# Kernel optimization log

Measured on AMD Instinct MI355X. Metric: run time of the kernel, lower is better.

Reference implementation:

```python
import jax, jax.numpy as jnp
import numpy as np

K = 3  # Chebyshev filter size (max_view)


def avwgcn(X, E, weights_pool, bias_pool):
    """Adaptive node-wise graph conv. X: [B,N,C_in], E: [N,D]."""
    N = E.shape[0]
    # adaptive adjacency: softmax over rows of relu(E E^T)
    supports = jax.nn.softmax(jax.nn.relu(E @ E.T), axis=1)  # [N,N]
    support_set = [jnp.eye(N, dtype=X.dtype), supports]
    for _ in range(2, K):  # Chebyshev recursion
        support_set.append(2.0 * supports @ support_set[-1] - support_set[-2])
    S = jnp.stack(support_set, axis=0)  # [K,N,N]
    W = jnp.einsum('nd,dkio->nkio', E, weights_pool)  # per-node weights [N,K,Ci,Co]
    bias = E @ bias_pool  # [N,Co]
    XG = jnp.einsum('knm,bmc->bnkc', S, X)  # [B,N,K,Ci]
    return jnp.einsum('bnki,nkio->bno', XG, W) + bias  # [B,N,Co]


def setup_inputs() -> dict:
    key = jax.random.key(0)
    ks = jax.random.split(key, 5)
    B, N, Cin, Cout, D = 32, 4096, 2, 64, 10
    Ci = Cin + Cout  # 66
    X = jax.random.normal(ks[0], (B, N, Cin), dtype=jnp.float32)
    H = jnp.zeros((B, N, Cout), dtype=jnp.float32)
    E = jax.random.normal(ks[1], (N, D), dtype=jnp.float32)
    W_gate = jax.random.normal(ks[2], (D, K, Ci, 2 * Cout), dtype=jnp.float32) * 0.1
    b_gate = jnp.zeros((D, 2 * Cout), dtype=jnp.float32)
    W_update = jax.random.normal(ks[3], (D, K, Ci, Cout), dtype=jnp.float32) * 0.1
    b_update = jnp.zeros((D, Cout), dtype=jnp.float32)
    return {"X": X, "H": H, "E": E, "W_gate": W_gate, "b_gate": b_gate,
            "W_update": W_update, "b_update": b_update}


def reference(X, H, E, W_gate, b_gate, W_update, b_update):
    Cout = H.shape[-1]
    XH = jnp.concatenate([X, H], axis=-1)  # [B,N,Cin+Cout]
    ZR = jax.nn.sigmoid(avwgcn(XH, E, W_gate, b_gate))  # [B,N,2*Cout]
    Z, R = ZR[..., :Cout], ZR[..., Cout:]
    C = jnp.concatenate([X, Z * H], axis=-1)
    HC = jnp.tanh(avwgcn(C, E, W_update, b_update))
    return R * H + (1.0 - R) * HC
```

## Files before the change

kernel.cpp:

```cpp
#include <hip/hip_runtime.h>
#include <math.h>

#define N_NODES 4096
#define BATCH   32
#define D_EMB   10
#define CIN     2
#define COUT    64
#define CI      66
#define KSUP    3
#define NCOLS   2112
#define NPAD    2176
#define LDT     4096

#define KI_REAL 198
#define KILD    232
#define OCH     (32 * KILD)
#define WROW_G  (128 * KILD)
#define WROW_U  (64 * KILD)
#define WGT2_R  (WROW_G + WROW_U)

typedef _Float16 half_t;
typedef __attribute__((ext_vector_type(8))) _Float16 f16x8;
typedef __attribute__((ext_vector_type(4))) _Float16 f16x4;
typedef __attribute__((ext_vector_type(2))) _Float16 f16x2;
typedef __attribute__((ext_vector_type(4))) float f32x4;

union u32h2 { unsigned u; f16x2 h; };

__device__ __forceinline__ float fast_sigmoid(float x) { return 1.f / (1.f + __expf(-x)); }
__device__ __forceinline__ float fast_tanh(float x) { return 1.f - 2.f / (__expf(2.f * x) + 1.f); }

__device__ __forceinline__ void gld_lds16(const half_t* g, half_t* l) {
  __builtin_amdgcn_global_load_lds(
      (const __attribute__((address_space(1))) void*)g,
      (__attribute__((address_space(3))) void*)l, 16, 0, 0);
}

__global__ __launch_bounds__(256) void k_softmax_p(const float* __restrict__ E,
                                                   half_t* __restrict__ Pb) {
  const int n = blockIdx.x;
  const int tid = threadIdx.x;
  __shared__ float En[D_EMB];
  __shared__ float ms[256], ss[256];
  if (tid < D_EMB) En[tid] = E[n * D_EMB + tid];
  __syncthreads();
  float en[D_EMB];
#pragma unroll
  for (int d = 0; d < D_EMB; ++d) en[d] = En[d];

  float m = -1e30f, s = 0.f;
  for (int c = tid; c < N_NODES; c += 256) {
    const float* Ec = E + c * D_EMB;
    float v = 0.f;
#pragma unroll
    for (int d = 0; d < D_EMB; ++d) v += en[d] * Ec[d];
    v = fmaxf(v, 0.f);
    if (v > m) { s *= __expf(m - v); m = v; }
    s += __expf(v - m);
  }
  ms[tid] = m; ss[tid] = s;
  __syncthreads();
  for (int off = 128; off > 0; off >>= 1) {
    if (tid < off) {
      float m2 = ms[tid + off], s2 = ss[tid + off];
      float m1 = ms[tid], s1 = ss[tid];
      float mm = fmaxf(m1, m2);
      ms[tid] = mm;
      ss[tid] = s1 * __expf(m1 - mm) + s2 * __expf(m2 - mm);
    }
    __syncthreads();
  }
  const float M = ms[0];
  const float inv = 1.f / ss[0];
  half_t* Pr = Pb + (size_t)n * N_NODES;
  for (int c = tid; c < N_NODES; c += 256) {
    const float* Ec = E + c * D_EMB;
    float v = 0.f;
#pragma unroll
    for (int d = 0; d < D_EMB; ++d) v += en[d] * Ec[d];
    v = fmaxf(v, 0.f);
    Pr[c] = (half_t)(__expf(v - M) * inv);
  }
}

__global__ __launch_bounds__(256) void k_build_v0(const float* __restrict__ X,
                                                  const float* __restrict__ H,
                                                  half_t* __restrict__ Vt,
                                                  half_t* __restrict__ Vn,
                                                  half_t* __restrict__ Cbt,
                                                  half_t* __restrict__ Cbn) {
  size_t idx = (size_t)blockIdx.x * 256 + threadIdx.x;
  if (idx >= (size_t)N_NODES * NCOLS) return;
  const int m = (int)(idx / NCOLS);
  const int col = (int)(idx % NCOLS);
  const int b = col / CI;
  const int c = col % CI;
  float v;
  if (c < CIN) v = X[((size_t)b * N_NODES + m) * CIN + c];
  else         v = H[((size_t)b * N_NODES + m) * COUT + (c - CIN)];
  const half_t h = (half_t)v;
  Vn[(size_t)m * NPAD + col] = h;
  Vt[(size_t)col * LDT + m] = h;
  if (c < CIN) {
    Cbn[(size_t)m * NPAD + col] = h;
    Cbt[(size_t)col * LDT + m] = h;
  }
}

__device__ __forceinline__ void gemm_compute_tile(const half_t* __restrict__ Lb,
                                                  int wm, int wn, int fofs,
                                                  f32x4 (&acc)[4][4]) {
  const half_t* As_ = Lb;
  const half_t* Bs_ = Lb + 4096;
  f16x8 a[4], b[4];
#pragma unroll
  for (int i = 0; i < 4; ++i)
    a[i] = *(const f16x8*)&As_[((wm >> 4) + i) * 512 + fofs];
#pragma unroll
  for (int j = 0; j < 4; ++j)
    b[j] = *(const f16x8*)&Bs_[((wn >> 4) + j) * 512 + fofs];
  __builtin_amdgcn_s_setprio(1);
#pragma unroll
  for (int i = 0; i < 4; ++i)
#pragma unroll
    for (int j = 0; j < 4; ++j)
      acc[i][j] = __builtin_amdgcn_mfma_f32_16x16x32_f16(a[i], b[j], acc[i][j], 0, 0, 0);
  __builtin_amdgcn_s_setprio(0);
}

__global__ __launch_bounds__(256) void k_gemm_f16(const half_t* __restrict__ A,
                                                  const half_t* __restrict__ Bt,
                                                  half_t* __restrict__ Cn,
                                                  half_t* __restrict__ Ct) {
  __shared__ half_t LB[3][8192];
  const int tid = threadIdx.x;
  const int lane = tid & 63;
  const int wave = tid >> 6;

  int flat = blockIdx.y * 17 + blockIdx.x;
  flat = (flat & 7) * 68 + (flat >> 3);
  const int bx = flat % 17;
  const int by = flat / 17;

  const int wm = (wave >> 1) * 64;
  const int wn = (wave & 1) * 64;
  const int rb = by * 128;
  const int cb = bx * 128;

  const int srow = lane >> 2;
  const int skg = (((lane & 3) + ((lane >> 3) & 3)) & 3) * 8;
  const half_t* ga0 = A + (size_t)(rb + wave * 32 + srow) * N_NODES + skg;
  const half_t* ga1 = ga0 + (size_t)16 * N_NODES;
  const half_t* gb0 = Bt + (size_t)(cb + wave * 32 + srow) * LDT + skg;
  const half_t* gb1 = gb0 + (size_t)16 * LDT;
  const int lA0 = wave * 1024;
  const int lA1 = lA0 + 512;
  const int lB0 = 4096 + wave * 1024;
  const int lB1 = lB0 + 512;

  const int fr = lane & 15;
  const int fg = lane >> 4;
  const int fofs = (4 * fr + ((fg - (fr >> 1)) & 3)) * 8;

  f32x4 acc[4][4] = {};

#define STAGE_T(buf, kk) do { half_t* Lp = LB[(buf)]; \
    gld_lds16(ga0 + (kk), Lp + lA0); gld_lds16(ga1 + (kk), Lp + lA1); \
    gld_lds16(gb0 + (kk), Lp + lB0); gld_lds16(gb1 + (kk), Lp + lB1); } while (0)

  STAGE_T(0, 0);
  STAGE_T(1, 32);

  for (int t = 0; t < 126; t += 3) {
    asm volatile("s_waitcnt vmcnt(4)\n\ts_barrier" ::: "memory");
    STAGE_T(2, (t + 2) * 32);
    gemm_compute_tile(LB[0], wm, wn, fofs, acc);

    asm volatile("s_waitcnt vmcnt(4)\n\ts_barrier" ::: "memory");
    STAGE_T(0, (t + 3) * 32);
    gemm_compute_tile(LB[1], wm, wn, fofs, acc);

    asm volatile("s_waitcnt vmcnt(4)\n\ts_barrier" ::: "memory");
    STAGE_T(1, (t + 4) * 32);
    gemm_compute_tile(LB[2], wm, wn, fofs, acc);
  }
  asm volatile("s_waitcnt vmcnt(4)\n\ts_barrier" ::: "memory");
  gemm_compute_tile(LB[0], wm, wn, fofs, acc);
  asm volatile("s_waitcnt vmcnt(0)\n\ts_barrier" ::: "memory");
  gemm_compute_tile(LB[1], wm, wn, fofs, acc);
#undef STAGE_T

  const int en = lane & 15;
  const int em = (lane >> 4) * 4;
#pragma unroll
  for (int i = 0; i < 4; ++i) {
#pragma unroll
    for (int j = 0; j < 4; ++j) {
      const int m0 = rb + wm + i * 16 + em;
      const int n = cb + wn + j * 16 + en;
      half_t h0 = (half_t)acc[i][j][0];
      half_t h1 = (half_t)acc[i][j][1];
      half_t h2 = (half_t)acc[i][j][2];
      half_t h3 = (half_t)acc[i][j][3];
      if (Ct) {
        f16x4 t4 = {h0, h1, h2, h3};
        *(f16x4*)&Ct[(size_t)n * LDT + m0] = t4;
      }
      Cn[(size_t)(m0 + 0) * NPAD + n] = h0;
      Cn[(size_t)(m0 + 1) * NPAD + n] = h1;
      Cn[(size_t)(m0 + 2) * NPAD + n] = h2;
      Cn[(size_t)(m0 + 3) * NPAD + n] = h3;
    }
  }
}

__global__ __launch_bounds__(256) void k_wgt2(const float* __restrict__ Wg,
                                              const float* __restrict__ Wu,
                                              unsigned* __restrict__ WT2) {
  const int r = blockIdx.x * 256 + threadIdx.x;
  if (r >= WGT2_R) return;
  const float* pool;
  int o, ki, ostr;
  if (r < WROW_G) { o = r / KILD; ki = r % KILD; pool = Wg; ostr = 128; }
  else { int r2 = r - WROW_G; o = r2 / KILD; ki = r2 % KILD; pool = Wu; ostr = 64; }
#pragma unroll
  for (int dp = 0; dp < 5; ++dp) {
    u32h2 v; v.h = f16x2{(half_t)0.f, (half_t)0.f};
    if (ki < KI_REAL) {
      const int k = ki / CI;
      const int i = ki % CI;
      v.h[0] = (half_t)pool[(((size_t)(2 * dp) * KSUP + k) * CI + i) * ostr + o];
      v.h[1] = (half_t)pool[(((size_t)(2 * dp + 1) * KSUP + k) * CI + i) * ostr + o];
    }
    WT2[(size_t)dp * WGT2_R + r] = v.u;
  }
}

__device__ __forceinline__ void stage_xg(const half_t* __restrict__ v0r,
                                         const half_t* __restrict__ g1r,
                                         const half_t* __restrict__ g2r,
                                         half_t* __restrict__ xg, int tid) {
  for (int idx = tid; idx < NCOLS / 8; idx += 256) {
    const f16x8 v0 = *(const f16x8*)&v0r[idx * 8];
    const f16x8 g1 = *(const f16x8*)&g1r[idx * 8];
    const f16x8 g2 = *(const f16x8*)&g2r[idx * 8];
    const f16x8 x2 = g2 + g2 - v0;
#pragma unroll
    for (int e = 0; e < 8; ++e) {
      const int col = idx * 8 + e;
      const int b = col / CI;
      const int i = col - b * CI;
      xg[b * KILD + i] = v0[e];
      xg[b * KILD + CI + i] = g1[e];
      xg[b * KILD + 2 * CI + i] = x2[e];
    }
  }
  for (int z = tid; z < 32 * 17; z += 256) {
    const int b = z / 17;
    const int j = z - b * 17;
    *(unsigned*)&xg[b * KILD + KI_REAL + j * 2] = 0u;
  }
}

__global__ __launch_bounds__(256) void k_gate_t(const half_t* __restrict__ Vn,
                                                const half_t* __restrict__ G1n,
                                                const half_t* __restrict__ G2n,
                                                const unsigned* __restrict__ WT2,
                                                const float* __restrict__ E,
                                                const float* __restrict__ bg,
                                                const float* __restrict__ H,
                                                half_t* __restrict__ Cbn,
                                                half_t* __restrict__ Cbt,
                                                half_t* __restrict__ Rb) {
  const int n0 = blockIdx.x * 2;
  const int tid = threadIdx.x;
  const int lane = tid & 63;
  const int wave = tid >> 6;
  __shared__ half_t Wl[2][OCH];
  __shared__ half_t xg[2][OCH];
  __shared__ float biasl[2][128];

  f16x2 e2p0[5], e2p1[5];
#pragma unroll
  for (int dp = 0; dp < 5; ++dp) {
    e2p0[dp][0] = (half_t)E[n0 * D_EMB + 2 * dp];
    e2p0[dp][1] = (half_t)E[n0 * D_EMB + 2 * dp + 1];
    e2p1[dp][0] = (half_t)E[(n0 + 1) * D_EMB + 2 * dp];
    e2p1[dp][1] = (half_t)E[(n0 + 1) * D_EMB + 2 * dp + 1];
  }

  {
    const int nn = tid >> 7;
    const int o = tid & 127;
    float s = 0.f;
#pragma unroll
    for (int d = 0; d < D_EMB; ++d) s += E[(n0 + nn) * D_EMB + d] * bg[d * 128 + o];
    biasl[nn][o] = s;
  }
  stage_xg(Vn + (size_t)n0 * NPAD, G1n + (size_t)n0 * NPAD, G2n + (size_t)n0 * NPAD, xg[0], tid);
  stage_xg(Vn + (size_t)(n0 + 1) * NPAD, G1n + (size_t)(n0 + 1) * NPAD, G2n + (size_t)(n0 + 1) * NPAD, xg[1], tid);

  const int fr = lane & 15;
  const int fk = (lane >> 4) * 8;
  const int en = lane & 15;
  const int em = (lane >> 4) * 4;
  const int node = wave & 1;
  const int ot = wave >> 1;
  const int nn = n0 + node;

#pragma unroll
  for (int p = 0; p < 4; ++p) {
    if (p > 0) __syncthreads();
    for (int base = tid * 8; base < OCH; base += 2048) {
      float a0[8] = {}, a1[8] = {};
#pragma unroll
      for (int dp = 0; dp < 5; ++dp) {
        const unsigned* wrow = WT2 + (size_t)dp * WGT2_R + p * OCH + base;
        uint4 wa = *(const uint4*)wrow;
        uint4 wb = *(const uint4*)(wrow + 4);
        u32h2 c0, c1, c2, c3;
        c0.u = wa.x; c1.u = wa.y; c2.u = wa.z; c3.u = wa.w;
        a0[0] = __builtin_amdgcn_fdot2(c0.h, e2p0[dp], a0[0], false);
        a0[1] = __builtin_amdgcn_fdot2(c1.h, e2p0[dp], a0[1], false);
        a0[2] = __builtin_amdgcn_fdot2(c2.h, e2p0[dp], a0[2], false);
        a0[3] = __builtin_amdgcn_fdot2(c3.h, e2p0[dp], a0[3], false);
        a1[0] = __builtin_amdgcn_fdot2(c0.h, e2p1[dp], a1[0], false);
        a1[1] = __builtin_amdgcn_fdot2(c1.h, e2p1[dp], a1[1], false);
        a1[2] = __builtin_amdgcn_fdot2(c2.h, e2p1[dp], a1[2], false);
        a1[3] = __builtin_amdgcn_fdot2(c3.h, e2p1[dp], a1[3], false);
        c0.u = wb.x; c1.u = wb.y; c2.u = wb.z; c3.u = wb.w;
        a0[4] = __builtin_amdgcn_fdot2(c0.h, e2p0[dp], a0[4], false);
        a0[5] = __builtin_amdgcn_fdot2(c1.h, e2p0[dp], a0[5], false);
        a0[6] = __builtin_amdgcn_fdot2(c2.h, e2p0[dp], a0[6], false);
        a0[7] = __builtin_amdgcn_fdot2(c3.h, e2p0[dp], a0[7], false);
        a1[4] = __builtin_amdgcn_fdot2(c0.h, e2p1[dp], a1[4], false);
        a1[5] = __builtin_amdgcn_fdot2(c1.h, e2p1[dp], a1[5], false);
        a1[6] = __builtin_amdgcn_fdot2(c2.h, e2p1[dp], a1[6], false);
        a1[7] = __builtin_amdgcn_fdot2(c3.h, e2p1[dp], a1[7], false);
      }
      f16x8 w0, w1;
#pragma unroll
      for (int e = 0; e < 8; ++e) { w0[e] = (half_t)a0[e]; w1[e] = (half_t)a1[e]; }
      *(f16x8*)&Wl[0][base] = w0;
      *(f16x8*)&Wl[1][base] = w1;
    }
    __syncthreads();

    f32x4 acc2[2] = {};
#pragma unroll
    for (int ks = 0; ks < 7; ++ks) {
      const f16x8 a0 = *(const f16x8*)&xg[node][fr * KILD + ks * 32 + fk];
      const f16x8 a1 = *(const f16x8*)&xg[node][(16 + fr) * KILD + ks * 32 + fk];
      const f16x8 b0 = *(const f16x8*)&Wl[node][(ot * 16 + fr) * KILD + ks * 32 + fk];
      acc2[0] = __builtin_amdgcn_mfma_f32_16x16x32_f16(a0, b0, acc2[0], 0, 0, 0);
      acc2[1] = __builtin_amdgcn_mfma_f32_16x16x32_f16(a1, b0, acc2[1], 0, 0, 0);
    }
    const int o_g = p * 32 + ot * 16 + en;
    const float bo = biasl[node][o_g];
#pragma unroll
    for (int i = 0; i < 2; ++i)
#pragma unroll
      for (int r = 0; r < 4; ++r) {
        const int b = i * 16 + em + r;
        const float s = fast_sigmoid(acc2[i][r] + bo);
        if (p < 2) {
          const float hv = H[((size_t)b * N_NODES + nn) * COUT + o_g];
          const half_t z = (half_t)(s * hv);
          const int c0 = b * CI + CIN + o_g;
          Cbn[(size_t)nn * NPAD + c0] = z;
          Cbt[(size_t)c0 * LDT + nn] = z;
        } else {
          Rb[((size_t)b * N_NODES + nn) * COUT + (o_g - 64)] = (half_t)s;
        }
      }
  }
}

__global__ __launch_bounds__(256) void k_update_t(const half_t* __restrict__ Cbn,
                                                  const half_t* __restrict__ G1n,
                                                  const half_t* __restrict__ G2n,
                                                  const unsigned* __restrict__ WT2,
                                                  const float* __restrict__ E,
                                                  const float* __restrict__ bu,
                                                  const float* __restrict__ H,
                                                  const half_t* __restrict__ Rb,
                                                  float* __restrict__ Out) {
  const int n0 = blockIdx.x * 2;
  const int tid = threadIdx.x;
  const int lane = tid & 63;
  const int wave = tid >> 6;
  __shared__ half_t Wl[2][OCH];
  __shared__ half_t xg[2][OCH];
  __shared__ float biasl[2][64];

  f16x2 e2p0[5], e2p1[5];
#pragma unroll
  for (int dp = 0; dp < 5; ++dp) {
    e2p0[dp][0] = (half_t)E[n0 * D_EMB + 2 * dp];
    e2p0[dp][1] = (half_t)E[n0 * D_EMB + 2 * dp + 1];
    e2p1[dp][0] = (half_t)E[(n0 + 1) * D_EMB + 2 * dp];
    e2p1[dp][1] = (half_t)E[(n0 + 1) * D_EMB + 2 * dp + 1];
  }

  if (tid < 128) {
    const int nn = tid >> 6;
    const int o = tid & 63;
    float s = 0.f;
#pragma unroll
    for (int d = 0; d < D_EMB; ++d) s += E[(n0 + nn) * D_EMB + d] * bu[d * COUT + o];
    biasl[nn][o] = s;
  }
  stage_xg(Cbn + (size_t)n0 * NPAD, G1n + (size_t)n0 * NPAD, G2n + (size_t)n0 * NPAD, xg[0], tid);
  stage_xg(Cbn + (size_t)(n0 + 1) * NPAD, G1n + (size_t)(n0 + 1) * NPAD, G2n + (size_t)(n0 + 1) * NPAD, xg[1], tid);

  const int fr = lane & 15;
  const int fk = (lane >> 4) * 8;
  const int en = lane & 15;
  const int em = (lane >> 4) * 4;
  const int node = wave & 1;
  const int ot = wave >> 1;
  const int nn = n0 + node;

#pragma unroll
  for (int p = 0; p < 2; ++p) {
    if (p > 0) __syncthreads();
    for (int base = tid * 8; base < OCH; base += 2048) {
      float a0[8] = {}, a1[8] = {};
#pragma unroll
      for (int dp = 0; dp < 5; ++dp) {
        const unsigned* wrow = WT2 + (size_t)dp * WGT2_R + WROW_G + p * OCH + base;
        uint4 wa = *(const uint4*)wrow;
        uint4 wb = *(const uint4*)(wrow + 4);
        u32h2 c0, c1, c2, c3;
        c0.u = wa.x; c1.u = wa.y; c2.u = wa.z; c3.u = wa.w;
        a0[0] = __builtin_amdgcn_fdot2(c0.h, e2p0[dp], a0[0], false);
        a0[1] = __builtin_amdgcn_fdot2(c1.h, e2p0[dp], a0[1], false);
        a0[2] = __builtin_amdgcn_fdot2(c2.h, e2p0[dp], a0[2], false);
        a0[3] = __builtin_amdgcn_fdot2(c3.h, e2p0[dp], a0[3], false);
        a1[0] = __builtin_amdgcn_fdot2(c0.h, e2p1[dp], a1[0], false);
        a1[1] = __builtin_amdgcn_fdot2(c1.h, e2p1[dp], a1[1], false);
        a1[2] = __builtin_amdgcn_fdot2(c2.h, e2p1[dp], a1[2], false);
        a1[3] = __builtin_amdgcn_fdot2(c3.h, e2p1[dp], a1[3], false);
        c0.u = wb.x; c1.u = wb.y; c2.u = wb.z; c3.u = wb.w;
        a0[4] = __builtin_amdgcn_fdot2(c0.h, e2p0[dp], a0[4], false);
        a0[5] = __builtin_amdgcn_fdot2(c1.h, e2p0[dp], a0[5], false);
        a0[6] = __builtin_amdgcn_fdot2(c2.h, e2p0[dp], a0[6], false);
        a0[7] = __builtin_amdgcn_fdot2(c3.h, e2p0[dp], a0[7], false);
        a1[4] = __builtin_amdgcn_fdot2(c0.h, e2p1[dp], a1[4], false);
        a1[5] = __builtin_amdgcn_fdot2(c1.h, e2p1[dp], a1[5], false);
        a1[6] = __builtin_amdgcn_fdot2(c2.h, e2p1[dp], a1[6], false);
        a1[7] = __builtin_amdgcn_fdot2(c3.h, e2p1[dp], a1[7], false);
      }
      f16x8 w0, w1;
#pragma unroll
      for (int e = 0; e < 8; ++e) { w0[e] = (half_t)a0[e]; w1[e] = (half_t)a1[e]; }
      *(f16x8*)&Wl[0][base] = w0;
      *(f16x8*)&Wl[1][base] = w1;
    }
    __syncthreads();

    f32x4 acc2[2] = {};
#pragma unroll
    for (int ks = 0; ks < 7; ++ks) {
      const f16x8 a0 = *(const f16x8*)&xg[node][fr * KILD + ks * 32 + fk];
      const f16x8 a1 = *(const f16x8*)&xg[node][(16 + fr) * KILD + ks * 32 + fk];
      const f16x8 b0 = *(const f16x8*)&Wl[node][(ot * 16 + fr) * KILD + ks * 32 + fk];
      acc2[0] = __builtin_amdgcn_mfma_f32_16x16x32_f16(a0, b0, acc2[0], 0, 0, 0);
      acc2[1] = __builtin_amdgcn_mfma_f32_16x16x32_f16(a1, b0, acc2[1], 0, 0, 0);
    }
    const int o = p * 32 + ot * 16 + en;
    const float bo = biasl[node][o];
#pragma unroll
    for (int i = 0; i < 2; ++i)
#pragma unroll
      for (int r = 0; r < 4; ++r) {
        const int b = i * 16 + em + r;
        const float hc = fast_tanh(acc2[i][r] + bo);
        const size_t base = ((size_t)b * N_NODES + nn) * COUT + o;
        const float hv = H[base];
        const float rr = (float)Rb[base];
        Out[base] = rr * hv + (1.f - rr) * hc;
      }
  }
}

extern "C" void kernel_launch(void* const* d_in, const int* in_sizes, int n_in,
                              void* d_out, int out_size, void* d_ws, size_t ws_size,
                              hipStream_t stream) {
  const float* X  = (const float*)d_in[0];
  const float* H  = (const float*)d_in[1];
  const float* E  = (const float*)d_in[2];
  const float* Wg = (const float*)d_in[3];
  const float* bg = (const float*)d_in[4];
  const float* Wu = (const float*)d_in[5];
  const float* bu = (const float*)d_in[6];
  float* out = (float*)d_out;

  const size_t SZ_P = (size_t)N_NODES * N_NODES;
  const size_t SZ_M = (size_t)NPAD * LDT;
  half_t* Pb  = (half_t*)d_ws;
  half_t* Vt  = Pb + SZ_P;
  half_t* Vn  = Vt + SZ_M;
  half_t* G1t = Vn + SZ_M;
  half_t* G1n = G1t + SZ_M;
  half_t* G2n = G1n + SZ_M;
  half_t* Cbt = G2n + SZ_M;
  half_t* Cbn = Cbt + SZ_M;
  half_t* Rb  = Cbn + SZ_M;
  unsigned* WT2 = (unsigned*)(Rb + (size_t)BATCH * N_NODES * COUT);

  k_softmax_p<<<N_NODES, 256, 0, stream>>>(E, Pb);
  {
    const size_t tot = (size_t)N_NODES * NCOLS;
    k_build_v0<<<(int)((tot + 255) / 256), 256, 0, stream>>>(X, H, Vt, Vn, Cbt, Cbn);
  }
  k_wgt2<<<(WGT2_R + 255) / 256, 256, 0, stream>>>(Wg, Wu, WT2);

  dim3 gg(NPAD / 128, N_NODES / 128);
  k_gemm_f16<<<gg, 256, 0, stream>>>(Pb, Vt, G1n, G1t);
  k_gemm_f16<<<gg, 256, 0, stream>>>(Pb, G1t, G2n, nullptr);
  k_gate_t<<<N_NODES / 2, 256, 0, stream>>>(Vn, G1n, G2n, WT2, E, bg, H, Cbn, Cbt, Rb);
  k_gemm_f16<<<gg, 256, 0, stream>>>(Pb, Cbt, G1n, G1t);
  k_gemm_f16<<<gg, 256, 0, stream>>>(Pb, G1t, G2n, nullptr);
  k_update_t<<<N_NODES / 2, 256, 0, stream>>>(Cbn, G1n, G2n, WT2, E, bu, H, Rb, out);
}
```

Baseline: 802.8 us.

## Vectorize xg staging with 72-wide K sections and double gate/update block size

Reorders the per-node K dimension into three 72-wide sections (66 real plus padding), so staging the Chebyshev inputs into shared memory uses 8-half vector loads and stores instead of scattered scalar writes. The weight-transpose kernel is changed to match the new K layout. The gate and update kernels now run 512 threads per block, and each wave computes one 16-batch half of the MFMA tile rather than both halves. This spreads the weight-generation and MFMA work across more waves at the cost of higher register and LDS pressure per block.

```diff
diff --git a/kernel.cpp b/kernel.cpp
--- a/kernel.cpp
+++ b/kernel.cpp
@@ -12,7 +12,8 @@
 #define NPAD    2176
 #define LDT     4096
 
-#define KI_REAL 198
+#define KSEC    72
+#define KI_REAL 216
 #define KILD    232
 #define OCH     (32 * KILD)
 #define WROW_G  (128 * KILD)
@@ -26,6 +27,13 @@
 typedef __attribute__((ext_vector_type(4))) float f32x4;
 
 union u32h2 { unsigned u; f16x2 h; };
+
+struct __attribute__((packed, aligned(4))) uint4_u4 { uint4 v; };
+__device__ __forceinline__ f16x8 loadu8h(const half_t* p) {
+  union { uint4 u; f16x8 h; } r;
+  r.u = ((const uint4_u4*)p)->v;
+  return r.h;
+}
 
 __device__ __forceinline__ float fast_sigmoid(float x) { return 1.f / (1.f + __expf(-x)); }
 __device__ __forceinline__ float fast_tanh(float x) { return 1.f - 2.f / (__expf(2.f * x) + 1.f); }
@@ -223,12 +231,12 @@
   int o, ki, ostr;
   if (r < WROW_G) { o = r / KILD; ki = r % KILD; pool = Wg; ostr = 128; }
   else { int r2 = r - WROW_G; o = r2 / KILD; ki = r2 % KILD; pool = Wu; ostr = 64; }
+  const int k = ki / KSEC;
+  const int i = ki - k * KSEC;
 #pragma unroll
   for (int dp = 0; dp < 5; ++dp) {
     u32h2 v; v.h = f16x2{(half_t)0.f, (half_t)0.f};
-    if (ki < KI_REAL) {
-      const int k = ki / CI;
-      const int i = ki % CI;
+    if (ki < KI_REAL && i < CI) {
       v.h[0] = (half_t)pool[(((size_t)(2 * dp) * KSUP + k) * CI + i) * ostr + o];
       v.h[1] = (half_t)pool[(((size_t)(2 * dp + 1) * KSUP + k) * CI + i) * ostr + o];
     }
@@ -239,30 +247,44 @@
 __device__ __forceinline__ void stage_xg(const half_t* __restrict__ v0r,
                                          const half_t* __restrict__ g1r,
                                          const half_t* __restrict__ g2r,
-                                         half_t* __restrict__ xg, int tid) {
-  for (int idx = tid; idx < NCOLS / 8; idx += 256) {
-    const f16x8 v0 = *(const f16x8*)&v0r[idx * 8];
-    const f16x8 g1 = *(const f16x8*)&g1r[idx * 8];
-    const f16x8 g2 = *(const f16x8*)&g2r[idx * 8];
-    const f16x8 x2 = g2 + g2 - v0;
-#pragma unroll
-    for (int e = 0; e < 8; ++e) {
-      const int col = idx * 8 + e;
-      const int b = col / CI;
-      const int i = col - b * CI;
-      xg[b * KILD + i] = v0[e];
-      xg[b * KILD + CI + i] = g1[e];
-      xg[b * KILD + 2 * CI + i] = x2[e];
-    }
-  }
-  for (int z = tid; z < 32 * 17; z += 256) {
-    const int b = z / 17;
-    const int j = z - b * 17;
-    *(unsigned*)&xg[b * KILD + KI_REAL + j * 2] = 0u;
-  }
-}
-
-__global__ __launch_bounds__(256) void k_gate_t(const half_t* __restrict__ Vn,
+                                         half_t* __restrict__ xg, int tid, int nthr) {
+  for (int w = tid; w < 32 * 9; w += nthr) {
+    const int b = w / 9;
+    const int oct = w - b * 9;
+    half_t* row = xg + b * KILD;
+    const half_t* pv = v0r + b * CI;
+    const half_t* pg1 = g1r + b * CI;
+    const half_t* pg2 = g2r + b * CI;
+    if (oct < 8) {
+      const f16x8 v0 = loadu8h(pv + oct * 8);
+      const f16x8 g1 = loadu8h(pg1 + oct * 8);
+      const f16x8 g2 = loadu8h(pg2 + oct * 8);
+      const f16x8 x2 = g2 + g2 - v0;
+      *(f16x8*)&row[oct * 8] = v0;
+      *(f16x8*)&row[KSEC + oct * 8] = g1;
+      *(f16x8*)&row[2 * KSEC + oct * 8] = x2;
+    } else {
+      u32h2 tv, tg1, tg2;
+      tv.u = *(const unsigned*)(pv + 64);
+      tg1.u = *(const unsigned*)(pg1 + 64);
+      tg2.u = *(const unsigned*)(pg2 + 64);
+      f16x8 v0 = {}, g1 = {}, x2 = {};
+      v0[0] = tv.h[0]; v0[1] = tv.h[1];
+      g1[0] = tg1.h[0]; g1[1] = tg1.h[1];
+      x2[0] = tg2.h[0] + tg2.h[0] - tv.h[0];
+      x2[1] = tg2.h[1] + tg2.h[1] - tv.h[1];
+      *(f16x8*)&row[64] = v0;
+      *(f16x8*)&row[KSEC + 64] = g1;
+      *(f16x8*)&row[2 * KSEC + 64] = x2;
+    }
+  }
+  for (int w = tid; w < 32 * 2; w += nthr) {
+    const f16x8 z = {};
+    *(f16x8*)&xg[(w >> 1) * KILD + KI_REAL + (w & 1) * 8] = z;
+  }
+}
+
+__global__ __launch_bounds__(512) void k_gate_t(const half_t* __restrict__ Vn,
                                                 const half_t* __restrict__ G1n,
                                                 const half_t* __restrict__ G2n,
                                                 const unsigned* __restrict__ WT2,
@@ -289,7 +311,7 @@
     e2p1[dp][1] = (half_t)E[(n0 + 1) * D_EMB + 2 * dp + 1];
   }
 
-  {
+  if (tid < 256) {
     const int nn = tid >> 7;
     const int o = tid & 127;
     float s = 0.f;
@@ -297,21 +319,22 @@
     for (int d = 0; d < D_EMB; ++d) s += E[(n0 + nn) * D_EMB + d] * bg[d * 128 + o];
     biasl[nn][o] = s;
   }
-  stage_xg(Vn + (size_t)n0 * NPAD, G1n + (size_t)n0 * NPAD, G2n + (size_t)n0 * NPAD, xg[0], tid);
-  stage_xg(Vn + (size_t)(n0 + 1) * NPAD, G1n + (size_t)(n0 + 1) * NPAD, G2n + (size_t)(n0 + 1) * NPAD, xg[1], tid);
+  stage_xg(Vn + (size_t)n0 * NPAD, G1n + (size_t)n0 * NPAD, G2n + (size_t)n0 * NPAD, xg[0], tid, 512);
+  stage_xg(Vn + (size_t)(n0 + 1) * NPAD, G1n + (size_t)(n0 + 1) * NPAD, G2n + (size_t)(n0 + 1) * NPAD, xg[1], tid, 512);
 
   const int fr = lane & 15;
   const int fk = (lane >> 4) * 8;
   const int en = lane & 15;
   const int em = (lane >> 4) * 4;
   const int node = wave & 1;
-  const int ot = wave >> 1;
+  const int ot = (wave >> 1) & 1;
+  const int bh = wave >> 2;
   const int nn = n0 + node;
 
 #pragma unroll
   for (int p = 0; p < 4; ++p) {
     if (p > 0) __syncthreads();
-    for (int base = tid * 8; base < OCH; base += 2048) {
+    for (int base = tid * 8; base < OCH; base += 4096) {
       float a0[8] = {}, a1[8] = {};
 #pragma unroll
       for (int dp = 0; dp < 5; ++dp) {
@@ -346,37 +369,33 @@
     }
     __syncthreads();
 
-    f32x4 acc2[2] = {};
+    f32x4 acc2 = {};
 #pragma unroll
     for (int ks = 0; ks < 7; ++ks) {
-      const f16x8 a0 = *(const f16x8*)&xg[node][fr * KILD + ks * 32 + fk];
-      const f16x8 a1 = *(const f16x8*)&xg[node][(16 + fr) * KILD + ks * 32 + fk];
+      const f16x8 a0 = *(const f16x8*)&xg[node][(bh * 16 + fr) * KILD + ks * 32 + fk];
       const f16x8 b0 = *(const f16x8*)&Wl[node][(ot * 16 + fr) * KILD + ks * 32 + fk];
-      acc2[0] = __builtin_amdgcn_mfma_f32_16x16x32_f16(a0, b0, acc2[0], 0, 0, 0);
-      acc2[1] = __builtin_amdgcn_mfma_f32_16x16x32_f16(a1, b0, acc2[1], 0, 0, 0);
+      acc2 = __builtin_amdgcn_mfma_f32_16x16x32_f16(a0, b0, acc2, 0, 0, 0);
     }
     const int o_g = p * 32 + ot * 16 + en;
     const float bo = biasl[node][o_g];
 #pragma unroll
-    for (int i = 0; i < 2; ++i)
-#pragma unroll
-      for (int r = 0; r < 4; ++r) {
-        const int b = i * 16 + em + r;
-        const float s = fast_sigmoid(acc2[i][r] + bo);
-        if (p < 2) {
-          const float hv = H[((size_t)b * N_NODES + nn) * COUT + o_g];
-          const half_t z = (half_t)(s * hv);
-          const int c0 = b * CI + CIN + o_g;
-          Cbn[(size_t)nn * NPAD + c0] = z;
-          Cbt[(size_t)c0 * LDT + nn] = z;
-        } else {
-          Rb[((size_t)b * N_NODES + nn) * COUT + (o_g - 64)] = (half_t)s;
-        }
+    for (int r = 0; r < 4; ++r) {
+      const int b = bh * 16 + em + r;
+      const float s = fast_sigmoid(acc2[r] + bo);
+      if (p < 2) {
+        const float hv = H[((size_t)b * N_NODES + nn) * COUT + o_g];
+        const half_t z = (half_t)(s * hv);
+        const int c0 = b * CI + CIN + o_g;
+        Cbn[(size_t)nn * NPAD + c0] = z;
+        Cbt[(size_t)c0 * LDT + nn] = z;
+      } else {
+        Rb[((size_t)b * N_NODES + nn) * COUT + (o_g - 64)] = (half_t)s;
       }
-  }
-}
-
-__global__ __launch_bounds__(256) void k_update_t(const half_t* __restrict__ Cbn,
+    }
+  }
+}
+
+__global__ __launch_bounds__(512) void k_update_t(const half_t* __restrict__ Cbn,
                                                   const half_t* __restrict__ G1n,
                                                   const half_t* __restrict__ G2n,
                                                   const unsigned* __restrict__ WT2,
@@ -410,21 +429,22 @@
     for (int d = 0; d < D_EMB; ++d) s += E[(n0 + nn) * D_EMB + d] * bu[d * COUT + o];
     biasl[nn][o] = s;
   }
-  stage_xg(Cbn + (size_t)n0 * NPAD, G1n + (size_t)n0 * NPAD, G2n + (size_t)n0 * NPAD, xg[0], tid);
-  stage_xg(Cbn + (size_t)(n0 + 1) * NPAD, G1n + (size_t)(n0 + 1) * NPAD, G2n + (size_t)(n0 + 1) * NPAD, xg[1], tid);
+  stage_xg(Cbn + (size_t)n0 * NPAD, G1n + (size_t)n0 * NPAD, G2n + (size_t)n0 * NPAD, xg[0], tid, 512);
+  stage_xg(Cbn + (size_t)(n0 + 1) * NPAD, G1n + (size_t)(n0 + 1) * NPAD, G2n + (size_t)(n0 + 1) * NPAD, xg[1], tid, 512);
 
   const int fr = lane & 15;
   const int fk = (lane >> 4) * 8;
   const int en = lane & 15;
   const int em = (lane >> 4) * 4;
   const int node = wave & 1;
-  const int ot = wave >> 1;
+  const int ot = (wave >> 1) & 1;
+  const int bh = wave >> 2;
   const int nn = n0 + node;
 
 #pragma unroll
   for (int p = 0; p < 2; ++p) {
     if (p > 0) __syncthreads();
-    for (int base = tid * 8; base < OCH; base += 2048) {
+    for (int base = tid * 8; base < OCH; base += 4096) {
       float a0[8] = {}, a1[8] = {};
 #pragma unroll
       for (int dp = 0; dp < 5; ++dp) {
@@ -459,28 +479,24 @@
     }
     __syncthreads();
 
-    f32x4 acc2[2] = {};
+    f32x4 acc2 = {};
 #pragma unroll
     for (int ks = 0; ks < 7; ++ks) {
-      const f16x8 a0 = *(const f16x8*)&xg[node][fr * KILD + ks * 32 + fk];
-      const f16x8 a1 = *(const f16x8*)&xg[node][(16 + fr) * KILD + ks * 32 + fk];
+      const f16x8 a0 = *(const f16x8*)&xg[node][(bh * 16 + fr) * KILD + ks * 32 + fk];
       const f16x8 b0 = *(const f16x8*)&Wl[node][(ot * 16 + fr) * KILD + ks * 32 + fk];
-      acc2[0] = __builtin_amdgcn_mfma_f32_16x16x32_f16(a0, b0, acc2[0], 0, 0, 0);
-      acc2[1] = __builtin_amdgcn_mfma_f32_16x16x32_f16(a1, b0, acc2[1], 0, 0, 0);
+      acc2 = __builtin_amdgcn_mfma_f32_16x16x32_f16(a0, b0, acc2, 0, 0, 0);
     }
     const int o = p * 32 + ot * 16 + en;
     const float bo = biasl[node][o];
 #pragma unroll
-    for (int i = 0; i < 2; ++i)
-#pragma unroll
-      for (int r = 0; r < 4; ++r) {
-        const int b = i * 16 + em + r;
-        const float hc = fast_tanh(acc2[i][r] + bo);
-        const size_t base = ((size_t)b * N_NODES + nn) * COUT + o;
-        const float hv = H[base];
-        const float rr = (float)Rb[base];
-        Out[base] = rr * hv + (1.f - rr) * hc;
-      }
+    for (int r = 0; r < 4; ++r) {
+      const int b = bh * 16 + em + r;
+      const float hc = fast_tanh(acc2[r] + bo);
+      const size_t base = ((size_t)b * N_NODES + nn) * COUT + o;
+      const float hv = H[base];
+      const float rr = (float)Rb[base];
+      Out[base] = rr * hv + (1.f - rr) * hc;
+    }
   }
 }
 
@@ -519,8 +535,8 @@
   dim3 gg(NPAD / 128, N_NODES / 128);
   k_gemm_f16<<<gg, 256, 0, stream>>>(Pb, Vt, G1n, G1t);
   k_gemm_f16<<<gg, 256, 0, stream>>>(Pb, G1t, G2n, nullptr);
-  k_gate_t<<<N_NODES / 2, 256, 0, stream>>>(Vn, G1n, G2n, WT2, E, bg, H, Cbn, Cbt, Rb);
+  k_gate_t<<<N_NODES / 2, 512, 0, stream>>>(Vn, G1n, G2n, WT2, E, bg, H, Cbn, Cbt, Rb);
   k_gemm_f16<<<gg, 256, 0, stream>>>(Pb, Cbt, G1n, G1t);
   k_gemm_f16<<<gg, 256, 0, stream>>>(Pb, G1t, G2n, nullptr);
-  k_update_t<<<N_NODES / 2, 256, 0, stream>>>(Cbn, G1n, G2n, WT2, E, bu, H, Rb, out);
-}
+  k_update_t<<<N_NODES / 2, 512, 0, stream>>>(Cbn, G1n, G2n, WT2, E, bu, H, Rb, out);
+}
```

New measurement: 790.9 us. No clear change (-1.5%).
